# Optimization experiments

Hardware: AMD Instinct MI355X
Metric: run time of the kernel (lower is better)

The kernel has to match this reference:

```python
import jax, jax.numpy as jnp
import numpy as np

# (multiplicity, irrep_dim) for irreps_in == irreps_out: 128x0e + 64x1o + 32x2e
IRREPS = [(128, 1), (64, 3), (32, 5)]
NUM_INDICES = 64
N_ELEMENTS = 8192
SCALE = 1.0  # module's `scale` arg; total coeff = scale / sqrt(num_indices) / sqrt(mul_in)
W_DIM = sum(m * m for m, _ in IRREPS)  # 21504


def setup_inputs() -> dict:
    key = jax.random.key(0)
    ks = jax.random.split(key, 5)
    x0 = jax.random.normal(ks[0], (N_ELEMENTS, 128, 1), jnp.float32)
    x1 = jax.random.normal(ks[1], (N_ELEMENTS, 64, 3), jnp.float32)
    x2 = jax.random.normal(ks[2], (N_ELEMENTS, 32, 5), jnp.float32)
    w = jax.random.normal(ks[3], (NUM_INDICES, W_DIM), jnp.float32)
    # Random contiguous segment sizes that sum exactly to N_ELEMENTS:
    bnd = jnp.sort(jax.random.randint(ks[4], (NUM_INDICES - 1,), 0, N_ELEMENTS + 1)).astype(jnp.int32)
    counts = jnp.diff(jnp.concatenate([jnp.zeros((1,), jnp.int32), bnd,
                                       jnp.full((1,), N_ELEMENTS, jnp.int32)]))
    return {"x0": x0, "x1": x1, "x2": x2, "w": w, "num_index_counts": counts}


def reference(x0, x1, x2, w, num_index_counts):
    """Indexed (segmented) equivariant linear: rows are grouped contiguously by
    num_index_counts; segment g uses weight row w[g]. Per matched irrep the
    weight block is a (mul_in, mul_out) mixing matrix applied identically to
    each of the ir.dim components (Schur's lemma), with fan-in normalization
    1/sqrt(mul_in) (cue.descriptors.linear) times scale/sqrt(num_indices)."""
    n = x0.shape[0]
    # segment id per row (rows are already grouped contiguously, as in Repeats())
    sid = jnp.repeat(jnp.arange(NUM_INDICES), num_index_counts, total_repeat_length=n)
    xs = (x0, x1, x2)
    ys = []
    off = 0
    for xk, (mul, ir_dim) in zip(xs, IRREPS):
        blk = w[:, off:off + mul * mul].reshape(NUM_INDICES, mul, mul)  # (E, m_in, m_out)
        coeff = float(SCALE / np.sqrt(NUM_INDICES) / np.sqrt(mul))
        wk = blk[sid]  # (n, m_in, m_out) per-row weight gather
        # y[n, o, i] = coeff * sum_m x[n, m, i] * w[g(n), m, o]
        ys.append(coeff * jnp.einsum('nmi,nmo->noi', xk, wk))
        off += mul * mul
    return tuple(ys)
```

## Files before the change

### kernel.cpp

```cpp
#include <hip/hip_runtime.h>

#define NSEG 64
#define NROW 8192
#define TILE 16
#define WROW 21504
#define NBPP 576
#define PT0 20
#define P1  196
#define P2  164

__global__ __launch_bounds__(256) void iil_kernel(
    const float* __restrict__ x0, const float* __restrict__ x1, const float* __restrict__ x2,
    const float* __restrict__ w, const int* __restrict__ counts,
    float* __restrict__ y0, float* __restrict__ y1, float* __restrict__ y2)
{
    __shared__ float sbuf[TILE * P1];
    __shared__ int sstart[NSEG + 1];
    __shared__ int tstart[NSEG + 1];

    const int t = threadIdx.x;

    if (t < NSEG) {
        int c = counts[t];
        int v = c;
        #pragma unroll
        for (int d = 1; d < NSEG; d <<= 1) {
            int u = __shfl_up(v, d, 64);
            if (t >= d) v += u;
        }
        sstart[t + 1] = v;
        int tc = (c + TILE - 1) >> 4;
        #pragma unroll
        for (int d = 1; d < NSEG; d <<= 1) {
            int u = __shfl_up(tc, d, 64);
            if (t >= d) tc += u;
        }
        tstart[t + 1] = tc;
        if (t == 0) { sstart[0] = 0; tstart[0] = 0; }
    }
    __syncthreads();

    const int phase = blockIdx.x / NBPP;
    const int pb = blockIdx.x - phase * NBPP;
    if (pb >= tstart[NSEG]) return;

    int lo = 0, hi = NSEG;
    while (hi - lo > 1) {
        int mid = (lo + hi) >> 1;
        if (tstart[mid] <= pb) lo = mid; else hi = mid;
    }
    const int g = lo;
    const int s = sstart[g] + (pb - tstart[g]) * TILE;
    const int nr = min(TILE, sstart[g + 1] - s);
    const float* __restrict__ wseg = w + (size_t)g * WROW;
    const float4 z4 = make_float4(0.f, 0.f, 0.f, 0.f);

    if (phase == 0) {
        float* xT0 = sbuf;
        const float4* g0 = (const float4*)x0 + (size_t)s * 32;
        #pragma unroll
        for (int i = 0; i < 2; ++i) {
            int idx = t + i * 256;
            int r = idx >> 5, c4 = idx & 31;
            float4 v = (r < nr) ? g0[idx] : z4;
            xT0[(c4 * 4 + 0) * PT0 + r] = v.x;
            xT0[(c4 * 4 + 1) * PT0 + r] = v.y;
            xT0[(c4 * 4 + 2) * PT0 + r] = v.z;
            xT0[(c4 * 4 + 3) * PT0 + r] = v.w;
        }
        __syncthreads();
        const int og = t & 31;
        const int rg = t >> 5;
        const float* wp = wseg + og * 4;
        const float* xb = xT0 + rg * 2;
        float acc[8];
        #pragma unroll
        for (int i = 0; i < 8; ++i) acc[i] = 0.f;
        #pragma unroll 8
        for (int k = 0; k < 128; ++k) {
            float2 xv = *(const float2*)(xb + k * PT0);
            float4 wv = *(const float4*)(wp + (size_t)k * 128);
            acc[0] = fmaf(xv.x, wv.x, acc[0]);
            acc[1] = fmaf(xv.x, wv.y, acc[1]);
            acc[2] = fmaf(xv.x, wv.z, acc[2]);
            acc[3] = fmaf(xv.x, wv.w, acc[3]);
            acc[4] = fmaf(xv.y, wv.x, acc[4]);
            acc[5] = fmaf(xv.y, wv.y, acc[5]);
            acc[6] = fmaf(xv.y, wv.z, acc[6]);
            acc[7] = fmaf(xv.y, wv.w, acc[7]);
        }
        const float c0 = 0.011048543456039806f;
        int r0 = rg * 2;
        if (r0 < nr)
            *(float4*)(y0 + (size_t)(s + r0) * 128 + og * 4) =
                make_float4(acc[0] * c0, acc[1] * c0, acc[2] * c0, acc[3] * c0);
        if (r0 + 1 < nr)
            *(float4*)(y0 + (size_t)(s + r0 + 1) * 128 + og * 4) =
                make_float4(acc[4] * c0, acc[5] * c0, acc[6] * c0, acc[7] * c0);
    } else if (phase == 1) {
        float* sx1 = sbuf;
        const float4* g1 = (const float4*)x1 + (size_t)s * 48;
        #pragma unroll
        for (int i = 0; i < 3; ++i) {
            int idx = t + i * 256;
            int r = idx / 48, c = idx - r * 48;
            float4 v = (r < nr) ? g1[idx] : z4;
            *(float4*)(sx1 + r * P1 + c * 4) = v;
        }
        __syncthreads();
        const int og = t & 15;
        const int r = t >> 4;
        const float* xrow = sx1 + r * P1;
        const float* wp = wseg + 16384 + og * 4;
        float acc[12];
        #pragma unroll
        for (int i = 0; i < 12; ++i) acc[i] = 0.f;
        #pragma unroll 2
        for (int kq = 0; kq < 16; ++kq) {
            float4 xq0 = *(const float4*)(xrow + 12 * kq + 0);
            float4 xq1 = *(const float4*)(xrow + 12 * kq + 4);
            float4 xq2 = *(const float4*)(xrow + 12 * kq + 8);
            float xf[12] = {xq0.x, xq0.y, xq0.z, xq0.w,
                            xq1.x, xq1.y, xq1.z, xq1.w,
                            xq2.x, xq2.y, xq2.z, xq2.w};
            #pragma unroll
            for (int kk = 0; kk < 4; ++kk) {
                float4 wv = *(const float4*)(wp + (size_t)(4 * kq + kk) * 64);
                #pragma unroll
                for (int oo = 0; oo < 4; ++oo) {
                    float wvo = (oo == 0) ? wv.x : (oo == 1) ? wv.y : (oo == 2) ? wv.z : wv.w;
                    acc[oo * 3 + 0] = fmaf(wvo, xf[kk * 3 + 0], acc[oo * 3 + 0]);
                    acc[oo * 3 + 1] = fmaf(wvo, xf[kk * 3 + 1], acc[oo * 3 + 1]);
                    acc[oo * 3 + 2] = fmaf(wvo, xf[kk * 3 + 2], acc[oo * 3 + 2]);
                }
            }
        }
        const float c1 = 0.015625f;
        if (r < nr) {
            float* yb = y1 + (size_t)(s + r) * 192 + og * 12;
            *(float4*)(yb + 0) = make_float4(acc[0] * c1, acc[1] * c1, acc[2] * c1, acc[3] * c1);
            *(float4*)(yb + 4) = make_float4(acc[4] * c1, acc[5] * c1, acc[6] * c1, acc[7] * c1);
            *(float4*)(yb + 8) = make_float4(acc[8] * c1, acc[9] * c1, acc[10] * c1, acc[11] * c1);
        }
    } else {
        float* sx2 = sbuf;
        const float4* g2 = (const float4*)x2 + (size_t)s * 40;
        #pragma unroll
        for (int i = 0; i < 3; ++i) {
            int idx = t + i * 256;
            if (idx < 640) {
                int r = idx / 40, c = idx - r * 40;
                float4 v = (r < nr) ? g2[idx] : z4;
                *(float4*)(sx2 + r * P2 + c * 4) = v;
            }
        }
        __syncthreads();
        const int og = t & 15;
        const int r = t >> 4;
        const float* xrow = sx2 + r * P2;
        const float* wp = wseg + 20480 + og * 2;
        float acc[10];
        #pragma unroll
        for (int i = 0; i < 10; ++i) acc[i] = 0.f;
        #pragma unroll
        for (int kq = 0; kq < 8; ++kq) {
            float xf[20];
            #pragma unroll
            for (int j = 0; j < 5; ++j) {
                float4 v = *(const float4*)(xrow + 20 * kq + 4 * j);
                xf[4 * j + 0] = v.x; xf[4 * j + 1] = v.y; xf[4 * j + 2] = v.z; xf[4 * j + 3] = v.w;
            }
            #pragma unroll
            for (int kk = 0; kk < 4; ++kk) {
                float2 wv = *(const float2*)(wp + (size_t)(4 * kq + kk) * 32);
                #pragma unroll
                for (int i = 0; i < 5; ++i) {
                    acc[i]     = fmaf(wv.x, xf[5 * kk + i], acc[i]);
                    acc[5 + i] = fmaf(wv.y, xf[5 * kk + i], acc[5 + i]);
                }
            }
        }
        const float c2 = 0.022097086912079608f;
        if (r < nr) {
            float* yb = y2 + (size_t)(s + r) * 160 + og * 10;
            #pragma unroll
            for (int i = 0; i < 5; ++i)
                *(float2*)(yb + 2 * i) = make_float2(acc[2 * i] * c2, acc[2 * i + 1] * c2);
        }
    }
}

extern "C" void kernel_launch(void* const* d_in, const int* in_sizes, int n_in,
                              void* d_out, int out_size, void* d_ws, size_t ws_size,
                              hipStream_t stream) {
    const float* x0 = (const float*)d_in[0];
    const float* x1 = (const float*)d_in[1];
    const float* x2 = (const float*)d_in[2];
    const float* w  = (const float*)d_in[3];
    const int* counts = (const int*)d_in[4];

    float* y0 = (float*)d_out;
    float* y1 = y0 + (size_t)NROW * 128;
    float* y2 = y1 + (size_t)NROW * 192;

    hipLaunchKernelGGL(iil_kernel, dim3(3 * NBPP), dim3(256), 0, stream,
                       x0, x1, x2, w, counts, y0, y1, y2);
}
```

Measured before the change: 96.59 us.

## Use 32-row tiles and a 4x4 register block for the scalar irrep phase

Phase 0 (the 128x0e block) now processes 32 rows per block instead of 16. Each thread computes 4 rows by 4 outputs, so every weight float4 load is reused across four rows and global weight traffic per output is cut. The x tile is now kept row-major with padding rather than transposed into shared memory. A separate tile prefix sum at 32-row granularity is added for this phase, so about half as many phase-0 blocks do work while the rest exit early, which trades parallelism for reuse.

```diff
diff --git a/kernel.cpp b/kernel.cpp
--- a/kernel.cpp
+++ b/kernel.cpp
@@ -2,21 +2,24 @@
 
 #define NSEG 64
 #define NROW 8192
-#define TILE 16
 #define WROW 21504
 #define NBPP 576
-#define PT0 20
-#define P1  196
-#define P2  164
+#define T0   32
+#define T12  16
+#define PX0  132
+#define P1   196
+#define P2   164
+#define SBUF_FLOATS 4224
 
 __global__ __launch_bounds__(256) void iil_kernel(
     const float* __restrict__ x0, const float* __restrict__ x1, const float* __restrict__ x2,
     const float* __restrict__ w, const int* __restrict__ counts,
     float* __restrict__ y0, float* __restrict__ y1, float* __restrict__ y2)
 {
-    __shared__ float sbuf[TILE * P1];
+    __shared__ float sbuf[SBUF_FLOATS];
     __shared__ int sstart[NSEG + 1];
-    __shared__ int tstart[NSEG + 1];
+    __shared__ int t16s[NSEG + 1];
+    __shared__ int t32s[NSEG + 1];
 
     const int t = threadIdx.x;
 
@@ -29,75 +32,114 @@
             if (t >= d) v += u;
         }
         sstart[t + 1] = v;
-        int tc = (c + TILE - 1) >> 4;
+        int a = (c + 15) >> 4;
         #pragma unroll
         for (int d = 1; d < NSEG; d <<= 1) {
-            int u = __shfl_up(tc, d, 64);
-            if (t >= d) tc += u;
-        }
-        tstart[t + 1] = tc;
-        if (t == 0) { sstart[0] = 0; tstart[0] = 0; }
+            int u = __shfl_up(a, d, 64);
+            if (t >= d) a += u;
+        }
+        t16s[t + 1] = a;
+        int b2 = (c + 31) >> 5;
+        #pragma unroll
+        for (int d = 1; d < NSEG; d <<= 1) {
+            int u = __shfl_up(b2, d, 64);
+            if (t >= d) b2 += u;
+        }
+        t32s[t + 1] = b2;
+        if (t == 0) { sstart[0] = 0; t16s[0] = 0; t32s[0] = 0; }
     }
     __syncthreads();
 
     const int phase = blockIdx.x / NBPP;
     const int pb = blockIdx.x - phase * NBPP;
-    if (pb >= tstart[NSEG]) return;
-
-    int lo = 0, hi = NSEG;
-    while (hi - lo > 1) {
-        int mid = (lo + hi) >> 1;
-        if (tstart[mid] <= pb) lo = mid; else hi = mid;
-    }
-    const int g = lo;
-    const int s = sstart[g] + (pb - tstart[g]) * TILE;
-    const int nr = min(TILE, sstart[g + 1] - s);
-    const float* __restrict__ wseg = w + (size_t)g * WROW;
     const float4 z4 = make_float4(0.f, 0.f, 0.f, 0.f);
 
     if (phase == 0) {
-        float* xT0 = sbuf;
+        if (pb >= t32s[NSEG]) return;
+        int lo = 0, hi = NSEG;
+        while (hi - lo > 1) {
+            int mid = (lo + hi) >> 1;
+            if (t32s[mid] <= pb) lo = mid; else hi = mid;
+        }
+        const int g = lo;
+        const int s = sstart[g] + (pb - t32s[g]) * T0;
+        const int nr = min(T0, sstart[g + 1] - s);
+        const float* __restrict__ wseg = w + (size_t)g * WROW;
+
         const float4* g0 = (const float4*)x0 + (size_t)s * 32;
         #pragma unroll
-        for (int i = 0; i < 2; ++i) {
+        for (int i = 0; i < 4; ++i) {
             int idx = t + i * 256;
             int r = idx >> 5, c4 = idx & 31;
             float4 v = (r < nr) ? g0[idx] : z4;
-            xT0[(c4 * 4 + 0) * PT0 + r] = v.x;
-            xT0[(c4 * 4 + 1) * PT0 + r] = v.y;
-            xT0[(c4 * 4 + 2) * PT0 + r] = v.z;
-            xT0[(c4 * 4 + 3) * PT0 + r] = v.w;
+            *(float4*)(sbuf + r * PX0 + c4 * 4) = v;
         }
         __syncthreads();
+
         const int og = t & 31;
         const int rg = t >> 5;
         const float* wp = wseg + og * 4;
-        const float* xb = xT0 + rg * 2;
-        float acc[8];
-        #pragma unroll
-        for (int i = 0; i < 8; ++i) acc[i] = 0.f;
-        #pragma unroll 8
-        for (int k = 0; k < 128; ++k) {
-            float2 xv = *(const float2*)(xb + k * PT0);
-            float4 wv = *(const float4*)(wp + (size_t)k * 128);
-            acc[0] = fmaf(xv.x, wv.x, acc[0]);
-            acc[1] = fmaf(xv.x, wv.y, acc[1]);
-            acc[2] = fmaf(xv.x, wv.z, acc[2]);
-            acc[3] = fmaf(xv.x, wv.w, acc[3]);
-            acc[4] = fmaf(xv.y, wv.x, acc[4]);
-            acc[5] = fmaf(xv.y, wv.y, acc[5]);
-            acc[6] = fmaf(xv.y, wv.z, acc[6]);
-            acc[7] = fmaf(xv.y, wv.w, acc[7]);
+        const float* xb = sbuf + rg * 4 * PX0;
+        float acc[16];
+        #pragma unroll
+        for (int i = 0; i < 16; ++i) acc[i] = 0.f;
+
+        #pragma unroll 2
+        for (int kq = 0; kq < 32; ++kq) {
+            const int k = kq * 4;
+            float4 xq0 = *(const float4*)(xb + 0 * PX0 + k);
+            float4 xq1 = *(const float4*)(xb + 1 * PX0 + k);
+            float4 xq2 = *(const float4*)(xb + 2 * PX0 + k);
+            float4 xq3 = *(const float4*)(xb + 3 * PX0 + k);
+            float4 w0q = *(const float4*)(wp + (size_t)(k + 0) * 128);
+            float4 w1q = *(const float4*)(wp + (size_t)(k + 1) * 128);
+            float4 w2q = *(const float4*)(wp + (size_t)(k + 2) * 128);
+            float4 w3q = *(const float4*)(wp + (size_t)(k + 3) * 128);
+#define RF(J, XQ)                                              \
+            acc[J*4+0] = fmaf(XQ.x, w0q.x, acc[J*4+0]);        \
+            acc[J*4+1] = fmaf(XQ.x, w0q.y, acc[J*4+1]);        \
+            acc[J*4+2] = fmaf(XQ.x, w0q.z, acc[J*4+2]);        \
+            acc[J*4+3] = fmaf(XQ.x, w0q.w, acc[J*4+3]);        \
+            acc[J*4+0] = fmaf(XQ.y, w1q.x, acc[J*4+0]);        \
+            acc[J*4+1] = fmaf(XQ.y, w1q.y, acc[J*4+1]);        \
+            acc[J*4+2] = fmaf(XQ.y, w1q.z, acc[J*4+2]);        \
+            acc[J*4+3] = fmaf(XQ.y, w1q.w, acc[J*4+3]);        \
+            acc[J*4+0] = fmaf(XQ.z, w2q.x, acc[J*4+0]);        \
+            acc[J*4+1] = fmaf(XQ.z, w2q.y, acc[J*4+1]);        \
+            acc[J*4+2] = fmaf(XQ.z, w2q.z, acc[J*4+2]);        \
+            acc[J*4+3] = fmaf(XQ.z, w2q.w, acc[J*4+3]);        \
+            acc[J*4+0] = fmaf(XQ.w, w3q.x, acc[J*4+0]);        \
+            acc[J*4+1] = fmaf(XQ.w, w3q.y, acc[J*4+1]);        \
+            acc[J*4+2] = fmaf(XQ.w, w3q.z, acc[J*4+2]);        \
+            acc[J*4+3] = fmaf(XQ.w, w3q.w, acc[J*4+3]);
+            RF(0, xq0)
+            RF(1, xq1)
+            RF(2, xq2)
+            RF(3, xq3)
+#undef RF
         }
         const float c0 = 0.011048543456039806f;
-        int r0 = rg * 2;
-        if (r0 < nr)
-            *(float4*)(y0 + (size_t)(s + r0) * 128 + og * 4) =
-                make_float4(acc[0] * c0, acc[1] * c0, acc[2] * c0, acc[3] * c0);
-        if (r0 + 1 < nr)
-            *(float4*)(y0 + (size_t)(s + r0 + 1) * 128 + og * 4) =
-                make_float4(acc[4] * c0, acc[5] * c0, acc[6] * c0, acc[7] * c0);
+        #pragma unroll
+        for (int j = 0; j < 4; ++j) {
+            int r = rg * 4 + j;
+            if (r < nr) {
+                *(float4*)(y0 + (size_t)(s + r) * 128 + og * 4) =
+                    make_float4(acc[j*4+0] * c0, acc[j*4+1] * c0,
+                                acc[j*4+2] * c0, acc[j*4+3] * c0);
+            }
+        }
     } else if (phase == 1) {
+        if (pb >= t16s[NSEG]) return;
+        int lo = 0, hi = NSEG;
+        while (hi - lo > 1) {
+            int mid = (lo + hi) >> 1;
+            if (t16s[mid] <= pb) lo = mid; else hi = mid;
+        }
+        const int g = lo;
+        const int s = sstart[g] + (pb - t16s[g]) * T12;
+        const int nr = min(T12, sstart[g + 1] - s);
+        const float* __restrict__ wseg = w + (size_t)g * WROW;
+
         float* sx1 = sbuf;
         const float4* g1 = (const float4*)x1 + (size_t)s * 48;
         #pragma unroll
@@ -108,6 +150,7 @@
             *(float4*)(sx1 + r * P1 + c * 4) = v;
         }
         __syncthreads();
+
         const int og = t & 15;
         const int r = t >> 4;
         const float* xrow = sx1 + r * P1;
@@ -143,6 +186,17 @@
             *(float4*)(yb + 8) = make_float4(acc[8] * c1, acc[9] * c1, acc[10] * c1, acc[11] * c1);
         }
     } else {
+        if (pb >= t16s[NSEG]) return;
+        int lo = 0, hi = NSEG;
+        while (hi - lo > 1) {
+            int mid = (lo + hi) >> 1;
+            if (t16s[mid] <= pb) lo = mid; else hi = mid;
+        }
+        const int g = lo;
+        const int s = sstart[g] + (pb - t16s[g]) * T12;
+        const int nr = min(T12, sstart[g + 1] - s);
+        const float* __restrict__ wseg = w + (size_t)g * WROW;
+
         float* sx2 = sbuf;
         const float4* g2 = (const float4*)x2 + (size_t)s * 40;
         #pragma unroll
@@ -155,6 +209,7 @@
             }
         }
         __syncthreads();
+
         const int og = t & 15;
         const int r = t >> 4;
         const float* xrow = sx2 + r * P2;
```

Measured after the change: 90.85 us. -5.9%, faster.
